# Kernel optimization log

Measured on AMD Instinct MI355X. Metric: run time of the kernel, lower is better.

## Reference

```python
import jax, jax.numpy as jnp
import numpy as np
from jax import lax

N_SEG = 196
EMB = 768
HID = 512
BN_EPS = 1e-5


def setup_inputs() -> dict:
    key = jax.random.key(0)
    ks = jax.random.split(key, 10)
    f32 = jnp.float32
    return {
        "img": jax.random.normal(ks[0], (8, 3, 224, 224), f32),
        "segments": jax.random.randint(ks[1], (8, 224, 224), 0, N_SEG).astype(jnp.int32),
        "conv1_w": jax.random.normal(ks[2], (64, 3, 7, 7), f32) * 0.05,
        "conv1_b": jnp.zeros((64,), f32),
        "bn1_g": jnp.ones((64,), f32),
        "bn1_b": jnp.zeros((64,), f32),
        "conv2_w": jax.random.normal(ks[3], (EMB, 64, 3, 3), f32) * 0.05,
        "conv2_b": jnp.zeros((EMB,), f32),
        "bn2_g": jnp.ones((EMB,), f32),
        "bn2_b": jnp.zeros((EMB,), f32),
        "pos_embed": jax.random.normal(ks[4], (N_SEG, EMB), f32),
        "W1": jax.random.normal(ks[5], (EMB, HID), f32) * 0.02,
        "b1": jax.random.normal(ks[6], (HID,), f32) * 0.001,
        "W2": jax.random.normal(ks[7], (HID, EMB), f32) * 0.02,
        "b2": jax.random.normal(ks[8], (EMB,), f32) * 0.001,
    }


def _conv(x, w, b, stride, pad):
    y = lax.conv_general_dilated(x, w, (stride, stride), [(pad, pad), (pad, pad)],
                                 dimension_numbers=("NCHW", "OIHW", "NCHW"))
    return y + b[None, :, None, None]


def _bn(x, g, b):
    # training-mode BatchNorm2d: batch stats over (B, H, W), biased variance
    mu = jnp.mean(x, axis=(0, 2, 3), keepdims=True)
    var = jnp.var(x, axis=(0, 2, 3), keepdims=True)
    return (x - mu) * lax.rsqrt(var + BN_EPS) * g[None, :, None, None] + b[None, :, None, None]


def reference(img, segments, conv1_w, conv1_b, bn1_g, bn1_b, conv2_w, conv2_b,
              bn2_g, bn2_b, pos_embed, W1, b1, W2, b2):
    # feature extractor: conv7x7/s2 -> BN -> ReLU -> conv3x3 -> BN -> ReLU
    f = jax.nn.relu(_bn(_conv(img, conv1_w, conv1_b, 2, 3), bn1_g, bn1_b))
    f = jax.nn.relu(_bn(_conv(f, conv2_w, conv2_b, 1, 1), bn2_g, bn2_b))  # [B,C,Hf,Wf]
    B, C, Hf, Wf = f.shape
    N = Hf * Wf

    # nearest-neighbor downsample of segment map to (Hf, Wf):
    # torch 'nearest': src = floor(dst * in/out)
    H, W = segments.shape[1], segments.shape[2]
    hi = (jnp.arange(Hf) * (H / Hf)).astype(jnp.int32)
    wi = (jnp.arange(Wf) * (W / Wf)).astype(jnp.int32)
    seg = jnp.take(jnp.take(segments, hi, axis=1), wi, axis=2)  # [B,Hf,Wf]
    seg_flat = seg.reshape(B * N)

    # NOTE: source does features.view(B, N, C) on an NCHW tensor (no permute);
    # faithfully replicate as a raw row-major reshape.
    feats = f.reshape(B * N, C)

    pos = pos_embed[seg_flat % N_SEG]  # [B*N, C]
    x = feats + pos

    # mask (segments >= 0) is all-true -> MaskedMLP reduces to a dense MLP
    h = jax.nn.gelu(x @ W1 + b1, approximate=False)  # [B*N, HID]
    y = h @ W2 + b2  # [B*N, C]

    gids = jnp.repeat(jnp.arange(B, dtype=jnp.int32), N) * N_SEG + seg_flat
    tokens = jnp.zeros((B * N_SEG, C), dtype=y.dtype).at[gids].set(y)
    return tokens.reshape(B, N_SEG, C)
```

## Files before the change

kernel.cpp:

```cpp
#include <hip/hip_runtime.h>
#include <hip/hip_bf16.h>

typedef __attribute__((ext_vector_type(4))) float f32x4;
typedef __attribute__((ext_vector_type(8))) short s16x8;
typedef __attribute__((ext_vector_type(4))) short s16x4;
typedef unsigned short u16;
typedef unsigned long long u64;

#define NB 8
#define NP 12544
#define PH 114
#define PP 12996
#define PPR 13056
#define QLIM 12768
#define NSEG 196
#define NTOK (NB*NSEG)
#define EMB 768
#define HID 512
#define AROWS 368
#define NBUCK 32

__device__ __forceinline__ u16 f2b(float v) {
  __hip_bfloat16 h = __float2bfloat16(v);
  return __builtin_bit_cast(u16, h);
}
__device__ __forceinline__ float b2f(u16 u) {
  unsigned int x = ((unsigned int)u) << 16;
  return __builtin_bit_cast(float, x);
}
__device__ __forceinline__ u16 f2h(float v) {
  _Float16 h = (_Float16)v;
  return __builtin_bit_cast(u16, h);
}
__device__ __forceinline__ float h2f(u16 u) {
  _Float16 h = __builtin_bit_cast(_Float16, u);
  return (float)h;
}
__device__ __forceinline__ u64 pack4h(f32x4 v) {
  s16x4 p;
#pragma unroll
  for (int e = 0; e < 4; ++e) p[e] = (short)f2h(v[e]);
  return __builtin_bit_cast(u64, p);
}

__device__ __forceinline__ void gl16(const u16* g, u16* l) {
  __builtin_amdgcn_global_load_lds((const __attribute__((address_space(1))) void*)g,
                                   (__attribute__((address_space(3))) void*)l, 16, 0, 0);
}

#define PR_WR1 (147 * 64)
#define PR_WR2 (9 * 768 * 64)
#define PR_W1T (512 * 768)
#define PR_W2T (768 * 512)
#define PR_LASTN (NB * NP)
__global__ void k_prep(const float* __restrict__ c1w, const float* __restrict__ c2w,
                       const float* __restrict__ W1, const float* __restrict__ W2,
                       const int* __restrict__ seg,
                       float* __restrict__ wr1, u16* __restrict__ wr2,
                       u16* __restrict__ w1t, u16* __restrict__ w2t,
                       int* __restrict__ lastn) {
  int id = blockIdx.x * 256 + threadIdx.x;
  if (id < PR_WR1) {
    int co = id & 63, k = id >> 6;
    int ci = k / 49, r = k % 49, kh = r / 7, kw = r % 7;
    wr1[k * 64 + co] = c1w[((co * 3 + ci) * 7 + kh) * 7 + kw];
    return;
  }
  id -= PR_WR1;
  if (id < PR_WR2) {
    int ci = id & 63, co = (id >> 6) % 768, tap = id / (64 * 768);
    int kh = tap / 3, kw = tap % 3;
    wr2[((size_t)(tap * 768 + co)) * 64 + ci] = f2b(c2w[((co * 64 + ci) * 3 + kh) * 3 + kw]);
    return;
  }
  id -= PR_WR2;
  if (id < PR_W1T) {
    int k = id % 768, n = id / 768;
    w1t[id] = f2b(W1[(size_t)k * 512 + n]);
    return;
  }
  id -= PR_W1T;
  if (id < PR_W2T) {
    int k = id % 512, n = id / 512;
    w2t[id] = f2b(W2[(size_t)k * 768 + n]);
    return;
  }
  id -= PR_W2T;
  if (id < PR_LASTN) {
    int b = id / NP, n = id % NP;
    int oh = n / 112, ow = n % 112;
    int s = seg[((size_t)b * 224 + oh * 2) * 224 + ow * 2];
    if ((unsigned)s < 196u) atomicMax(&lastn[b * NSEG + s], n);
  }
}

__global__ __launch_bounds__(256) void k_conv1(const float* __restrict__ img,
                                               const float* __restrict__ wr1,
                                               u16* __restrict__ c1,
                                               float* __restrict__ sumb,
                                               float* __restrict__ sqb) {
  int owt = blockIdx.x, oh = blockIdx.y, b = blockIdx.z;
  int t = threadIdx.x;
  __shared__ float xs[3 * 7 * 37];
  __shared__ float ls[64], lq[64];
  if (t < 64) { ls[t] = 0.f; lq[t] = 0.f; }
  int iw0 = owt * 32 - 3;
  int ih0 = oh * 2 - 3;
  for (int i = t; i < 3 * 7 * 37; i += 256) {
    int ci = i / (7 * 37), r = i % (7 * 37), kh = r / 37, cc = r % 37;
    int ih = ih0 + kh, iw = iw0 + cc;
    float v = 0.f;
    if ((unsigned)ih < 224u && (unsigned)iw < 224u)
      v = img[((size_t)(b * 3 + ci) * 224 + ih) * 224 + iw];
    xs[i] = v;
  }
  __syncthreads();
  int co = t & 63, g = t >> 6;
  float a0 = 0.f, a1 = 0.f, a2 = 0.f, a3 = 0.f;
  for (int ci = 0; ci < 3; ++ci)
    for (int kh = 0; kh < 7; ++kh) {
      const float* xrow = &xs[(ci * 7 + kh) * 37];
      const float* wrow = &wr1[(ci * 49 + kh * 7) * 64 + co];
#pragma unroll
      for (int kw = 0; kw < 7; ++kw) {
        float wv = wrow[kw * 64];
        int base = g * 8 + kw;
        a0 += xrow[base + 0] * wv;
        a1 += xrow[base + 2] * wv;
        a2 += xrow[base + 4] * wv;
        a3 += xrow[base + 6] * wv;
      }
    }
  size_t p0 = (size_t)b * NP + oh * 112 + owt * 16 + g * 4;
  c1[(p0 + 0) * 64 + co] = f2b(a0);
  c1[(p0 + 1) * 64 + co] = f2b(a1);
  c1[(p0 + 2) * 64 + co] = f2b(a2);
  c1[(p0 + 3) * 64 + co] = f2b(a3);
  float s = a0 + a1 + a2 + a3;
  float q = a0 * a0 + a1 * a1 + a2 * a2 + a3 * a3;
  atomicAdd(&ls[co], s);
  atomicAdd(&lq[co], q);
  __syncthreads();
  if (t < 64) {
    int bid = owt + 7 * (oh + 112 * b);
    int bk = (bid & (NBUCK - 1)) * 64 + t;
    atomicAdd(&sumb[bk], ls[t]);
    atomicAdd(&sqb[bk], lq[t]);
  }
}

__global__ void k_bncoef(const float* __restrict__ sumb, const float* __restrict__ sqb,
                         const float* __restrict__ g, const float* __restrict__ bb,
                         float* __restrict__ a, float* __restrict__ s, int C, float invN,
                         int nbuck) {
  int i = blockIdx.x * 256 + threadIdx.x;
  if (i >= C) return;
  float ms = 0.f, qs = 0.f;
  for (int k = 0; k < nbuck; ++k) { ms += sumb[k * C + i]; qs += sqb[k * C + i]; }
  float m = ms * invN;
  float v = qs * invN - m * m;
  float ai = g[i] * rsqrtf(v + 1e-5f);
  a[i] = ai;
  s[i] = bb[i] - m * ai;
}

__global__ __launch_bounds__(256, 2) void k_conv2_stats(const u16* __restrict__ c1,
                                                        const u16* __restrict__ wr2,
                                                        const float* __restrict__ a1,
                                                        const float* __restrict__ s1,
                                                        float* __restrict__ sum,
                                                        float* __restrict__ sq,
                                                        u16* __restrict__ y) {
  const int t = threadIdx.x;
  const int lane = t & 63;
  const int w = t >> 6;
  const int wr = w >> 1, wc = w & 1;
  const int h = blockIdx.x;
  const int b = h & 7;
  const int r8 = h >> 3;
  const int q0 = (r8 / 6) * 128;
  const int co0 = (r8 % 6) * 128;
  const int la = lane & 15, lb = lane >> 4;

  __shared__ __align__(16) u16 As[AROWS * 64];
  __shared__ __align__(16) u16 Bs[2][128 * 64];
  __shared__ float csum[128], csq[128];
  if (t < 128) { csum[t] = 0.f; csq[t] = 0.f; }

#define BSTAGE(tap, buf) do {                                                   \
    const u16* bsrc_ = wr2 + ((size_t)((tap) * 768 + co0)) * 64;                 \
    _Pragma("unroll")                                                            \
    for (int i_ = 0; i_ < 4; ++i_) {                                             \
      int s_ = i_ * 256 + w * 64 + lane;                                         \
      int r_ = s_ >> 3, c_ = s_ & 7;                                             \
      int cg_ = c_ ^ (r_ & 7);                                                   \
      gl16(bsrc_ + (size_t)r_ * 64 + cg_ * 8,                                    \
           &Bs[buf][(size_t)(i_ * 256 + w * 64) * 8]);                           \
    }                                                                            \
  } while (0)

  BSTAGE(0, 0);
  {
    const u16* c1b = c1 + (size_t)b * NP * 64;
    const int c = t & 7;
    f32x4 aLo = *(const f32x4*)&a1[c * 8];
    f32x4 aHi = *(const f32x4*)&a1[c * 8 + 4];
    f32x4 sLo = *(const f32x4*)&s1[c * 8];
    f32x4 sHi = *(const f32x4*)&s1[c * 8 + 4];
#pragma unroll
    for (int hh = 0; hh < 2; ++hh) {
      s16x8 vv[6];
      bool ok0, ok1, ok2, ok3, ok4, ok5;
#pragma unroll
      for (int i = 0; i < 6; ++i) {
        int s = (hh * 6 + i) * 256 + t;
        int r = s >> 3;
        int p = q0 + r;
        int pd = p / PH, pm = p - pd * PH;
        bool valid = (s < AROWS * 8) && (pd >= 1) && (pd <= 112) && (pm >= 1) && (pm <= 112);
        int pix = valid ? ((pd - 1) * 112 + (pm - 1)) : 0;
        vv[i] = *(const s16x8*)&c1b[(size_t)pix * 64 + c * 8];
        if (i == 0) ok0 = valid; else if (i == 1) ok1 = valid; else if (i == 2) ok2 = valid;
        else if (i == 3) ok3 = valid; else if (i == 4) ok4 = valid; else ok5 = valid;
      }
#pragma unroll
      for (int i = 0; i < 6; ++i) {
        int s = (hh * 6 + i) * 256 + t;
        if (s < AROWS * 8) {
          int r = s >> 3;
          bool valid = (i == 0) ? ok0 : (i == 1) ? ok1 : (i == 2) ? ok2
                     : (i == 3) ? ok3 : (i == 4) ? ok4 : ok5;
          s16x8 o = {0, 0, 0, 0, 0, 0, 0, 0};
          if (valid) {
            s16x8 v = vv[i];
#pragma unroll
            for (int e = 0; e < 4; ++e) {
              o[e]     = (short)f2b(fmaxf(aLo[e] * b2f((u16)v[e])     + sLo[e], 0.f));
              o[e + 4] = (short)f2b(fmaxf(aHi[e] * b2f((u16)v[e + 4]) + sHi[e], 0.f));
            }
          }
          *(s16x8*)&As[r * 64 + ((c ^ (r & 7)) * 8)] = o;
        }
      }
    }
  }
  __syncthreads();

  const f32x4 zero4 = {0.f, 0.f, 0.f, 0.f};
  f32x4 acc[4][4];
#pragma unroll
  for (int i = 0; i < 4; ++i)
#pragma unroll
    for (int j = 0; j < 4; ++j) acc[i][j] = zero4;

  for (int tap = 0; tap < 9; ++tap) {
    const int off = (tap / 3) * PH + (tap % 3);
    const int buf = tap & 1;

    s16x8 af[4][2], bf[4][2];
#pragma unroll
    for (int qf = 0; qf < 4; ++qf) {
      int r = wr * 64 + qf * 16 + la + off;
      int rx = r & 7;
#pragma unroll
      for (int ks = 0; ks < 2; ++ks) {
        int slot = (ks * 4 + lb) ^ rx;
        af[qf][ks] = *(const s16x8*)&As[r * 64 + slot * 8];
      }
    }
#pragma unroll
    for (int cf = 0; cf < 4; ++cf) {
      int r = wc * 64 + cf * 16 + la;
      int rx = r & 7;
#pragma unroll
      for (int ks = 0; ks < 2; ++ks) {
        int slot = (ks * 4 + lb) ^ rx;
        bf[cf][ks] = *(const s16x8*)&Bs[buf][r * 64 + slot * 8];
      }
    }

    if (tap < 8) BSTAGE(tap + 1, buf ^ 1);

#pragma unroll
    for (int ks = 0; ks < 2; ++ks)
#pragma unroll
      for (int qf = 0; qf < 4; ++qf)
#pragma unroll
        for (int cf = 0; cf < 4; ++cf)
          acc[qf][cf] = __builtin_amdgcn_mfma_f32_16x16x32_bf16(af[qf][ks], bf[cf][ks], acc[qf][cf], 0, 0, 0);

    __syncthreads();
  }
#undef BSTAGE

  u64* S = (u64*)As;
#pragma unroll
  for (int cf = 0; cf < 4; ++cf) {
    int row = wc * 64 + cf * 16 + la;
#pragma unroll
    for (int qf = 0; qf < 4; ++qf) {
      int chunk = wr * 16 + qf * 4 + lb;
      S[row * 32 + (chunk ^ (row & 15))] = pack4h(acc[qf][cf]);
    }
  }

  bool vmask[16];
#pragma unroll
  for (int qf = 0; qf < 4; ++qf)
#pragma unroll
    for (int rr = 0; rr < 4; ++rr) {
      int q = q0 + wr * 64 + qf * 16 + lb * 4 + rr;
      vmask[qf * 4 + rr] = (q < QLIM) && ((q % PH) < 112);
    }
#pragma unroll
  for (int cf = 0; cf < 4; ++cf) {
    const int cob = wc * 64 + cf * 16 + la;
    float s = 0.f, ss = 0.f;
#pragma unroll
    for (int qf = 0; qf < 4; ++qf)
#pragma unroll
      for (int rr = 0; rr < 4; ++rr) {
        float v = acc[qf][cf][rr];
        if (vmask[qf * 4 + rr]) { s += v; ss += v * v; }
      }
    s += __shfl_xor(s, 16); ss += __shfl_xor(ss, 16);
    s += __shfl_xor(s, 32); ss += __shfl_xor(ss, 32);
    if (lane < 16) { atomicAdd(&csum[cob], s); atomicAdd(&csq[cob], ss); }
  }
  __syncthreads();

  {
    const size_t ybb = ((size_t)b * EMB + co0) * PPR + q0;
#pragma unroll
    for (int i = 0; i < 16; ++i) {
      int g = i * 256 + t;
      int row = g >> 5, c = g & 31;
      u64 pk = S[row * 32 + (c ^ (row & 15))];
      *(u64*)&y[ybb + (size_t)row * PPR + c * 4] = pk;
    }
  }
  if (t < 128) { atomicAdd(&sum[co0 + t], csum[t]); atomicAdd(&sq[co0 + t], csq[t]); }
}

__global__ __launch_bounds__(256) void k_token_out(const u16* __restrict__ y,
                                                   const int* __restrict__ lastn,
                                                   const float* __restrict__ a2,
                                                   const float* __restrict__ s2,
                                                   const float* __restrict__ pos,
                                                   u16* __restrict__ x) {
  int tok = blockIdx.x;
  int b = tok / NSEG, sg = tok % NSEG;
  int n = lastn[tok];
  int t = threadIdx.x;
  for (int c = t; c < EMB; c += 256) {
    float r = 0.f;
    if (n >= 0) {
      int j = n * EMB + c;
      int ch = j / NP, sp = j - ch * NP;
      int qd = sp / 112, qm = sp - qd * 112;
      float v = h2f(y[((size_t)b * EMB + ch) * PPR + qd * PH + qm]);
      r = fmaxf(a2[ch] * v + s2[ch], 0.f) + pos[(size_t)sg * EMB + c];
    }
    x[(size_t)tok * EMB + c] = f2b(r);
  }
}

__global__ __launch_bounds__(256) void k_mlp1(const u16* __restrict__ x,
                                              const u16* __restrict__ w1t,
                                              const float* __restrict__ b1,
                                              u16* __restrict__ h) {
  int t = threadIdx.x, lane = t & 63, w = t >> 6;
  int la = lane & 15, lb = lane >> 4;
  int m0 = (blockIdx.x * 4 + w) * 16;
  int n0 = blockIdx.y * 64;
  const f32x4 zero4 = {0.f, 0.f, 0.f, 0.f};
  f32x4 acc[4] = {zero4, zero4, zero4, zero4};
  int mrow = m0 + la; if (mrow >= NTOK) mrow = NTOK - 1;
  for (int k = 0; k < EMB; k += 32) {
    int ko = k + lb * 8;
    s16x8 a = *(const s16x8*)(x + (size_t)mrow * EMB + ko);
#pragma unroll
    for (int cf = 0; cf < 4; ++cf) {
      s16x8 bv = *(const s16x8*)(w1t + (size_t)(n0 + cf * 16 + la) * EMB + ko);
      acc[cf] = __builtin_amdgcn_mfma_f32_16x16x32_bf16(a, bv, acc[cf], 0, 0, 0);
    }
  }
#pragma unroll
  for (int cf = 0; cf < 4; ++cf) {
    int n = n0 + cf * 16 + la;
    float bias = b1[n];
#pragma unroll
    for (int r = 0; r < 4; ++r) {
      int m = m0 + lb * 4 + r;
      if (m < NTOK) {
        float v = acc[cf][r] + bias;
        float gg = 0.5f * v * (1.f + erff(v * 0.70710678118654752f));
        h[(size_t)m * HID + n] = f2b(gg);
      }
    }
  }
}

__global__ __launch_bounds__(256) void k_mlp2(const u16* __restrict__ h,
                                              const u16* __restrict__ w2t,
                                              const float* __restrict__ b2,
                                              const int* __restrict__ lastn,
                                              float* __restrict__ out) {
  int t = threadIdx.x, lane = t & 63, w = t >> 6;
  int la = lane & 15, lb = lane >> 4;
  int m0 = (blockIdx.x * 4 + w) * 16;
  int n0 = blockIdx.y * 64;
  const f32x4 zero4 = {0.f, 0.f, 0.f, 0.f};
  f32x4 acc[4] = {zero4, zero4, zero4, zero4};
  int mrow = m0 + la; if (mrow >= NTOK) mrow = NTOK - 1;
  for (int k = 0; k < HID; k += 32) {
    int ko = k + lb * 8;
    s16x8 a = *(const s16x8*)(h + (size_t)mrow * HID + ko);
#pragma unroll
    for (int cf = 0; cf < 4; ++cf) {
      s16x8 bv = *(const s16x8*)(w2t + (size_t)(n0 + cf * 16 + la) * HID + ko);
      acc[cf] = __builtin_amdgcn_mfma_f32_16x16x32_bf16(a, bv, acc[cf], 0, 0, 0);
    }
  }
#pragma unroll
  for (int cf = 0; cf < 4; ++cf) {
    int n = n0 + cf * 16 + la;
    float bias = b2[n];
#pragma unroll
    for (int r = 0; r < 4; ++r) {
      int m = m0 + lb * 4 + r;
      if (m < NTOK)
        out[(size_t)m * EMB + n] = (lastn[m] >= 0) ? (acc[cf][r] + bias) : 0.f;
    }
  }
}

extern "C" void kernel_launch(void* const* d_in, const int* in_sizes, int n_in,
                              void* d_out, int out_size, void* d_ws, size_t ws_size,
                              hipStream_t stream) {
  const float* img  = (const float*)d_in[0];
  const int*   seg  = (const int*)  d_in[1];
  const float* c1w  = (const float*)d_in[2];
  const float* bn1g = (const float*)d_in[4];
  const float* bn1b = (const float*)d_in[5];
  const float* c2w  = (const float*)d_in[6];
  const float* bn2g = (const float*)d_in[8];
  const float* bn2b = (const float*)d_in[9];
  const float* pos  = (const float*)d_in[10];
  const float* W1   = (const float*)d_in[11];
  const float* b1   = (const float*)d_in[12];
  const float* W2   = (const float*)d_in[13];
  const float* b2   = (const float*)d_in[14];

  char* ws = (char*)d_ws;
  size_t off = 0;
  auto alloc = [&](size_t bytes) { size_t o = off; off = (off + bytes + 255) & ~(size_t)255; return o; };

  size_t oC1  = alloc((size_t)NB * NP * 64 * 2);
  size_t oY   = alloc((size_t)NB * EMB * PPR * 2);
  size_t oWr2 = alloc((size_t)9 * 768 * 64 * 2);
  size_t oWr1 = alloc(147 * 64 * 4);
  size_t oW1T = alloc((size_t)HID * EMB * 2);
  size_t oW2T = alloc((size_t)EMB * HID * 2);
  size_t oSum = alloc((NBUCK * 64 * 2 + 768 + 768) * 4);
  size_t oCoef = alloc((64 + 64 + 768 + 768) * 4);
  size_t oLast = alloc(NTOK * 4);
  size_t oX   = alloc((size_t)NTOK * EMB * 2);
  size_t oH   = alloc((size_t)NTOK * HID * 2);
  (void)ws_size; (void)in_sizes; (void)n_in;

  u16*   c1   = (u16*)(ws + oC1);
  u16*   y    = (u16*)(ws + oY);
  u16*   wr2  = (u16*)(ws + oWr2);
  float* wr1  = (float*)(ws + oWr1);
  u16*   w1t  = (u16*)(ws + oW1T);
  u16*   w2t  = (u16*)(ws + oW2T);
  float* bn1sumb = (float*)(ws + oSum);
  float* bn1sqb  = bn1sumb + NBUCK * 64;
  float* bn2sum  = bn1sumb + NBUCK * 64 * 2;
  float* bn2sq   = bn2sum + 768;
  float* a1 = (float*)(ws + oCoef);
  float* s1 = a1 + 64;
  float* a2 = a1 + 128;
  float* s2 = a2 + 768;
  int*   lastn = (int*)(ws + oLast);
  u16*   x  = (u16*)(ws + oX);
  u16*   h  = (u16*)(ws + oH);
  float* out = (float*)d_out;

  hipMemsetAsync(ws + oSum, 0, (NBUCK * 64 * 2 + 768 + 768) * 4, stream);
  hipMemsetAsync(ws + oLast, 0xFF, NTOK * 4, stream);

  const int prep_total = PR_WR1 + PR_WR2 + PR_W1T + PR_W2T + PR_LASTN;
  k_prep<<<(prep_total + 255) / 256, 256, 0, stream>>>(c1w, c2w, W1, W2, seg,
                                                        wr1, wr2, w1t, w2t, lastn);

  k_conv1<<<dim3(7, 112, 8), 256, 0, stream>>>(img, wr1, c1, bn1sumb, bn1sqb);
  k_bncoef<<<1, 256, 0, stream>>>(bn1sumb, bn1sqb, bn1g, bn1b, a1, s1, 64, 1.f / 100352.f, NBUCK);

  k_conv2_stats<<<4800, 256, 0, stream>>>(c1, wr2, a1, s1, bn2sum, bn2sq, y);
  k_bncoef<<<3, 256, 0, stream>>>(bn2sum, bn2sq, bn2g, bn2b, a2, s2, 768, 1.f / 100352.f, 1);

  k_token_out<<<NTOK, 256, 0, stream>>>(y, lastn, a2, s2, pos, x);

  k_mlp1<<<dim3(25, 8), 256, 0, stream>>>(x, w1t, b1, h);
  k_mlp2<<<dim3(25, 12), 256, 0, stream>>>(h, w2t, b2, lastn, out);
}
```

Before: 257.2 us.

## Load conv2 weight fragments directly into registers and drop LDS B staging

Conv2 weight fragments now go straight from global memory into registers, prefetched one tap ahead, instead of being staged through a double-buffered shared-memory tile. This removes the per-tap block barrier and 32KB of LDS. Occupancy is raised to 3 blocks per CU. In exchange each wave issues its own global loads, with some redundancy across the waves sharing a column, and register pressure rises, which may cause spills under the tighter launch bound.

```diff
diff --git a/kernel.cpp b/kernel.cpp
--- a/kernel.cpp
+++ b/kernel.cpp
@@ -41,11 +41,6 @@
 #pragma unroll
   for (int e = 0; e < 4; ++e) p[e] = (short)f2h(v[e]);
   return __builtin_bit_cast(u64, p);
-}
-
-__device__ __forceinline__ void gl16(const u16* g, u16* l) {
-  __builtin_amdgcn_global_load_lds((const __attribute__((address_space(1))) void*)g,
-                                   (__attribute__((address_space(3))) void*)l, 16, 0, 0);
 }
 
 #define PR_WR1 (147 * 64)
@@ -164,7 +159,7 @@
   s[i] = bb[i] - m * ai;
 }
 
-__global__ __launch_bounds__(256, 2) void k_conv2_stats(const u16* __restrict__ c1,
+__global__ __launch_bounds__(256, 3) void k_conv2_stats(const u16* __restrict__ c1,
                                                         const u16* __restrict__ wr2,
                                                         const float* __restrict__ a1,
                                                         const float* __restrict__ s1,
@@ -183,23 +178,20 @@
   const int la = lane & 15, lb = lane >> 4;
 
   __shared__ __align__(16) u16 As[AROWS * 64];
-  __shared__ __align__(16) u16 Bs[2][128 * 64];
   __shared__ float csum[128], csq[128];
   if (t < 128) { csum[t] = 0.f; csq[t] = 0.f; }
 
-#define BSTAGE(tap, buf) do {                                                   \
-    const u16* bsrc_ = wr2 + ((size_t)((tap) * 768 + co0)) * 64;                 \
-    _Pragma("unroll")                                                            \
-    for (int i_ = 0; i_ < 4; ++i_) {                                             \
-      int s_ = i_ * 256 + w * 64 + lane;                                         \
-      int r_ = s_ >> 3, c_ = s_ & 7;                                             \
-      int cg_ = c_ ^ (r_ & 7);                                                   \
-      gl16(bsrc_ + (size_t)r_ * 64 + cg_ * 8,                                    \
-           &Bs[buf][(size_t)(i_ * 256 + w * 64) * 8]);                           \
-    }                                                                            \
-  } while (0)
-
-  BSTAGE(0, 0);
+  const u16* bbase = wr2 + ((size_t)(co0 + wc * 64)) * 64 + lb * 8;
+#define LOADB(tap, dst)                                                         \
+  _Pragma("unroll")                                                             \
+  for (int cf_ = 0; cf_ < 4; ++cf_)                                             \
+    _Pragma("unroll")                                                           \
+    for (int ks_ = 0; ks_ < 2; ++ks_)                                           \
+      dst[cf_][ks_] = *(const s16x8*)(bbase + ((size_t)(tap) * 768 + cf_ * 16 + la) * 64 + ks_ * 32);
+
+  s16x8 bf[4][2], bn[4][2];
+  LOADB(0, bf);
+
   {
     const u16* c1b = c1 + (size_t)b * NP * 64;
     const int c = t & 7;
@@ -253,45 +245,38 @@
 #pragma unroll
     for (int j = 0; j < 4; ++j) acc[i][j] = zero4;
 
+#pragma unroll
   for (int tap = 0; tap < 9; ++tap) {
+    if (tap < 8) LOADB(tap + 1, bn);
     const int off = (tap / 3) * PH + (tap % 3);
-    const int buf = tap & 1;
-
-    s16x8 af[4][2], bf[4][2];
-#pragma unroll
-    for (int qf = 0; qf < 4; ++qf) {
-      int r = wr * 64 + qf * 16 + la + off;
-      int rx = r & 7;
-#pragma unroll
-      for (int ks = 0; ks < 2; ++ks) {
-        int slot = (ks * 4 + lb) ^ rx;
-        af[qf][ks] = *(const s16x8*)&As[r * 64 + slot * 8];
-      }
-    }
-#pragma unroll
-    for (int cf = 0; cf < 4; ++cf) {
-      int r = wc * 64 + cf * 16 + la;
-      int rx = r & 7;
-#pragma unroll
-      for (int ks = 0; ks < 2; ++ks) {
-        int slot = (ks * 4 + lb) ^ rx;
-        bf[cf][ks] = *(const s16x8*)&Bs[buf][r * 64 + slot * 8];
-      }
-    }
-
-    if (tap < 8) BSTAGE(tap + 1, buf ^ 1);
-
-#pragma unroll
-    for (int ks = 0; ks < 2; ++ks)
+
+#pragma unroll
+    for (int ks = 0; ks < 2; ++ks) {
+      s16x8 af[4];
+#pragma unroll
+      for (int qf = 0; qf < 4; ++qf) {
+        int r = wr * 64 + qf * 16 + la + off;
+        int slot = (ks * 4 + lb) ^ (r & 7);
+        af[qf] = *(const s16x8*)&As[r * 64 + slot * 8];
+      }
 #pragma unroll
       for (int qf = 0; qf < 4; ++qf)
 #pragma unroll
         for (int cf = 0; cf < 4; ++cf)
-          acc[qf][cf] = __builtin_amdgcn_mfma_f32_16x16x32_bf16(af[qf][ks], bf[cf][ks], acc[qf][cf], 0, 0, 0);
-
-    __syncthreads();
-  }
-#undef BSTAGE
+          acc[qf][cf] = __builtin_amdgcn_mfma_f32_16x16x32_bf16(af[qf], bf[cf][ks], acc[qf][cf], 0, 0, 0);
+    }
+
+    if (tap < 8) {
+#pragma unroll
+      for (int cf = 0; cf < 4; ++cf)
+#pragma unroll
+        for (int ks = 0; ks < 2; ++ks)
+          bf[cf][ks] = bn[cf][ks];
+    }
+  }
+#undef LOADB
+
+  __syncthreads();
 
   u64* S = (u64*)As;
 #pragma unroll
```

New measurement: 317.9 us. +23.6%, slower.
